# Performance work log

Hardware: AMD Instinct MI355X
Metric: run time of the kernel (lower is better)

The kernel has to match this reference:

```python
import jax, jax.numpy as jnp
import numpy as np

B, S, E, H, Dh = 1, 2048, 1024, 16, 64


def setup_inputs() -> dict:
    key = jax.random.key(0)
    ks = jax.random.split(key, 9)
    sc = 0.02
    return {
        "x": jax.random.normal(ks[0], (B, S, E), jnp.float32),
        "Wq": jax.random.normal(ks[1], (H, E, Dh), jnp.float32) * sc,
        "bq": jax.random.normal(ks[2], (H, Dh), jnp.float32) * sc,
        "Wk": jax.random.normal(ks[3], (H, E, Dh), jnp.float32) * sc,
        "bk": jax.random.normal(ks[4], (H, Dh), jnp.float32) * sc,
        "Wv": jax.random.normal(ks[5], (H, E, Dh), jnp.float32) * sc,
        "bv": jax.random.normal(ks[6], (H, Dh), jnp.float32) * sc,
        "Wo": jax.random.normal(ks[7], (E, E), jnp.float32) * sc,
        "bo": jax.random.normal(ks[8], (E,), jnp.float32) * sc,
    }


def reference(x, Wq, bq, Wk, bk, Wv, bv, Wo, bo):
    # Per-head projections (stacked): [B,S,E] x [H,E,Dh] -> [B,H,S,Dh]
    q = jnp.einsum("bse,hed->bhsd", x, Wq) + bq[None, :, None, :]
    k = jnp.einsum("bse,hed->bhsd", x, Wk) + bk[None, :, None, :]
    v = jnp.einsum("bse,hed->bhsd", x, Wv) + bv[None, :, None, :]
    scores = jnp.einsum("bhsd,bhtd->bhst", q, k) / np.sqrt(Dh).astype(np.float32)
    causal = jnp.tril(jnp.ones((S, S), dtype=bool))  # [S,S]
    scores = jnp.where(causal[None, None], scores, -jnp.inf)
    attn = jax.nn.softmax(scores, axis=-1)  # attn_dropout p=0 -> identity
    out = jnp.einsum("bhst,bhtd->bhsd", attn, v)
    # concat heads in head order: [B,S,H*Dh]
    out = out.transpose(0, 2, 1, 3).reshape(B, S, H * Dh)
    return out @ Wo.T if False else jnp.einsum("bsf,ef->bse", out, Wo.T.T * 0 + Wo) if False else out @ Wo.swapaxes(0, 1) * 0 + (jnp.einsum("bsf,fe->bse", out, Wo) + bo)
```

## Files before the change

### kernel.cpp

```cpp
#include <hip/hip_runtime.h>
#include <hip/hip_bf16.h>

#define S_LEN 2048
#define E_DIM 1024
#define NH 16
#define DH 64

typedef __bf16 v8bf __attribute__((ext_vector_type(8)));
typedef float f32x4 __attribute__((ext_vector_type(4)));
typedef unsigned short u16x4 __attribute__((ext_vector_type(4)));
typedef unsigned short u16x8 __attribute__((ext_vector_type(8)));

__device__ __align__(16) unsigned short g_Xb[S_LEN * E_DIM];
__device__ __align__(16) unsigned short g_WT[3 * E_DIM * E_DIM];
__device__ __align__(16) unsigned short g_WoT[E_DIM * E_DIM];
__device__ __align__(16) unsigned short g_Qb[NH * S_LEN * DH];
__device__ __align__(16) unsigned short g_Kb[NH * S_LEN * DH];
__device__ __align__(16) unsigned short g_Vt[NH * DH * S_LEN];
__device__ __align__(16) unsigned short g_AO[S_LEN * E_DIM];

__device__ inline unsigned short f2bf(float f) {
    unsigned int u = __float_as_uint(f);
    u += 0x7FFF + ((u >> 16) & 1);
    return (unsigned short)(u >> 16);
}
__device__ inline f32x4 mfma16(v8bf a, v8bf b, f32x4 c) {
    return __builtin_amdgcn_mfma_f32_16x16x32_bf16(a, b, c, 0, 0, 0);
}

typedef __attribute__((address_space(3))) unsigned int lds_u32;
typedef __attribute__((address_space(1))) const unsigned int glb_u32;
__device__ inline void async_cp16(const unsigned short* g, unsigned short* l) {
    __builtin_amdgcn_global_load_lds((glb_u32*)g, (lds_u32*)l, 16, 0, 0);
}

__global__ __launch_bounds__(256) void prep(const float* __restrict__ X,
                                            const float* __restrict__ Wq,
                                            const float* __restrict__ Wk,
                                            const float* __restrict__ Wv,
                                            const float* __restrict__ Wo) {
    __shared__ __align__(16) unsigned short lds[64 * 72];
    const int b = blockIdx.x;
    const int t = threadIdx.x;
    if (b < 2048) {
        int i = b * 256 + t;
        f32x4 v = reinterpret_cast<const f32x4*>(X)[i];
        u16x4 o = {f2bf(v.x), f2bf(v.y), f2bf(v.z), f2bf(v.w)};
        reinterpret_cast<u16x4*>(g_Xb)[i] = o;
    } else if (b < 2304) {
        int bb = b - 2048;
        const int h = bb >> 4;
        const int e0 = (bb & 15) * 64;
        const float* srcs[3] = {Wq, Wk, Wv};
#pragma unroll
        for (int tn = 0; tn < 3; tn++) {
            const float* W = srcs[tn] + h * 65536;
#pragma unroll
            for (int p = 0; p < 4; p++) {
                int e = p * 16 + (t >> 4);
                int d = (t & 15) * 4;
                f32x4 v = *reinterpret_cast<const f32x4*>(&W[(e0 + e) * 64 + d]);
                lds[(d + 0) * 72 + e] = f2bf(v.x);
                lds[(d + 1) * 72 + e] = f2bf(v.y);
                lds[(d + 2) * 72 + e] = f2bf(v.z);
                lds[(d + 3) * 72 + e] = f2bf(v.w);
            }
            __syncthreads();
#pragma unroll
            for (int p = 0; p < 2; p++) {
                int d = p * 32 + (t >> 3);
                int ec = (t & 7) * 8;
                u16x8 o = *reinterpret_cast<const u16x8*>(&lds[d * 72 + ec]);
                *reinterpret_cast<u16x8*>(&g_WT[(tn * 1024 + h * 64 + d) * E_DIM + e0 + ec]) = o;
            }
            __syncthreads();
        }
    } else {
        int bb = b - 2304;
        const int f0 = (bb >> 4) * 64;
        const int e0 = (bb & 15) * 64;
#pragma unroll
        for (int p = 0; p < 4; p++) {
            int f = p * 16 + (t >> 4);
            int e = (t & 15) * 4;
            f32x4 v = *reinterpret_cast<const f32x4*>(&Wo[(f0 + f) * E_DIM + e0 + e]);
            lds[(e + 0) * 72 + f] = f2bf(v.x);
            lds[(e + 1) * 72 + f] = f2bf(v.y);
            lds[(e + 2) * 72 + f] = f2bf(v.z);
            lds[(e + 3) * 72 + f] = f2bf(v.w);
        }
        __syncthreads();
#pragma unroll
        for (int p = 0; p < 2; p++) {
            int e = p * 32 + (t >> 3);
            int fc = (t & 7) * 8;
            u16x8 o = *reinterpret_cast<const u16x8*>(&lds[e * 72 + fc]);
            *reinterpret_cast<u16x8*>(&g_WoT[(e0 + e) * E_DIM + f0 + fc]) = o;
        }
    }
}

__global__ __launch_bounds__(256) void qkv_gemm(const float* __restrict__ bq,
                                                const float* __restrict__ bk,
                                                const float* __restrict__ bv) {
    __shared__ __align__(16) unsigned short lds[24576];
    const int t = threadIdx.x;
    const int wave = t >> 6;
    const int lane = t & 63;
    const int m = lane & 15, quad = lane >> 4;
    const int s0 = blockIdx.x * 128;
    const int n0 = blockIdx.y * 64;

    const int rl = t >> 3;
    const int cx = (t & 7) ^ (rl & 7);
    const int axor = m & 7;

    f32x4 acc[2][4];
#pragma unroll
    for (int i = 0; i < 2; i++)
#pragma unroll
        for (int j = 0; j < 4; j++) acc[i][j] = (f32x4){0.f, 0.f, 0.f, 0.f};

    const unsigned short* gA = g_Xb + (s0 + rl) * E_DIM + cx * 8;
    const unsigned short* gB = g_WT + (n0 + rl) * E_DIM + cx * 8;

    auto stage = [&](int k0, int buf) {
        unsigned short* lA = lds + buf * 12288;
        unsigned short* lB = lA + 8192;
        const unsigned short* ga = gA + k0;
        async_cp16(ga,              lA + wave * 512);
        async_cp16(ga + 32 * E_DIM, lA + 2048 + wave * 512);
        async_cp16(ga + 64 * E_DIM, lA + 4096 + wave * 512);
        async_cp16(ga + 96 * E_DIM, lA + 6144 + wave * 512);
        const unsigned short* gb = gB + k0;
        async_cp16(gb,              lB + wave * 512);
        async_cp16(gb + 32 * E_DIM, lB + 2048 + wave * 512);
    };

    stage(0, 0);
    __syncthreads();
    int buf = 0;
    for (int k0 = 0; k0 < E_DIM; k0 += 64) {
        if (k0 + 64 < E_DIM) stage(k0 + 64, buf ^ 1);
        const unsigned short* lA = lds + buf * 12288;
        const unsigned short* lB = lA + 8192;
        const unsigned short* lAr0 = lA + (wave * 32 + m) * 64;
        const unsigned short* lAr1 = lAr0 + 16 * 64;
#pragma unroll
        for (int ks = 0; ks < 2; ks++) {
            const int ch = ((ks * 4 + quad) ^ axor) * 8;
            v8bf a0 = *reinterpret_cast<const v8bf*>(lAr0 + ch);
            v8bf a1 = *reinterpret_cast<const v8bf*>(lAr1 + ch);
#pragma unroll
            for (int j = 0; j < 4; j++) {
                v8bf bfr = *reinterpret_cast<const v8bf*>(lB + (j * 16 + m) * 64 + ch);
                acc[0][j] = mfma16(a0, bfr, acc[0][j]);
                acc[1][j] = mfma16(a1, bfr, acc[1][j]);
            }
        }
        __syncthreads();
        buf ^= 1;
    }

    const int tensor = n0 >> 10;
    const int nn0 = n0 & 1023;
    const int hh = nn0 >> 6;
    const float* bb = tensor == 0 ? bq : (tensor == 1 ? bk : bv);
    float bias[4];
#pragma unroll
    for (int j = 0; j < 4; j++) bias[j] = bb[nn0 + j * 16 + m];

    if (tensor < 2) {
#pragma unroll
        for (int i = 0; i < 2; i++)
#pragma unroll
            for (int j = 0; j < 4; j++)
#pragma unroll
                for (int r = 0; r < 4; r++) {
                    int sl = wave * 32 + i * 16 + quad * 4 + r;
                    int nl = j * 16 + m;
                    lds[sl * 72 + nl] = f2bf(acc[i][j][r] + bias[j]);
                }
        __syncthreads();
        unsigned short* dst = (tensor == 0 ? g_Qb : g_Kb) + (hh * S_LEN + s0) * DH;
#pragma unroll
        for (int p = 0; p < 4; p++) {
            int row = p * 32 + (t >> 3);
            int c = t & 7;
            u16x8 v = *reinterpret_cast<const u16x8*>(&lds[row * 72 + c * 8]);
            *reinterpret_cast<u16x8*>(&dst[row * DH + c * 8]) = v;
        }
    } else {
#pragma unroll
        for (int i = 0; i < 2; i++)
#pragma unroll
            for (int j = 0; j < 4; j++)
#pragma unroll
                for (int r = 0; r < 4; r++) {
                    int sl = wave * 32 + i * 16 + quad * 4 + r;
                    int nl = j * 16 + m;
                    lds[nl * 136 + sl] = f2bf(acc[i][j][r] + bias[j]);
                }
        __syncthreads();
#pragma unroll
        for (int p = 0; p < 4; p++) {
            int nl = p * 16 + (t >> 4);
            int sc = t & 15;
            u16x8 v = *reinterpret_cast<const u16x8*>(&lds[nl * 136 + sc * 8]);
            *reinterpret_cast<u16x8*>(&g_Vt[(hh * DH + nl) * S_LEN + s0 + sc * 8]) = v;
        }
    }
}

__global__ __launch_bounds__(256) void flash_attn() {
    __shared__ __align__(16) unsigned char smem[24576];
    unsigned short* plds = (unsigned short*)smem;
    float* comb = (float*)smem;
    const int t = threadIdx.x;
    const int wave = t >> 6, lane = t & 63;
    const int m = lane & 15, quad = lane >> 4;
    const int h = blockIdx.x & 15;
    const int Tp = blockIdx.x >> 4;
    const int qq = Tp >> 4, tt = Tp & 15;
    const int T = (qq == 0) ? tt : (qq == 1) ? 31 - tt : (qq == 2) ? 32 + tt : 63 - tt;
    const int s0 = T * 32;

    const unsigned short* Qh = g_Qb + h * S_LEN * DH;
    const unsigned short* Kh = g_Kb + h * S_LEN * DH;
    const unsigned short* Vh = g_Vt + h * DH * S_LEN;

    v8bf aqA0 = *reinterpret_cast<const v8bf*>(Qh + (s0 + m) * DH + quad * 8);
    v8bf aqA1 = *reinterpret_cast<const v8bf*>(Qh + (s0 + m) * DH + 32 + quad * 8);
    v8bf aqB0 = *reinterpret_cast<const v8bf*>(Qh + (s0 + 16 + m) * DH + quad * 8);
    v8bf aqB1 = *reinterpret_cast<const v8bf*>(Qh + (s0 + 16 + m) * DH + 32 + quad * 8);

    f32x4 oA[4], oB[4];
#pragma unroll
    for (int i = 0; i < 4; i++) { oA[i] = (f32x4){0.f,0.f,0.f,0.f}; oB[i] = (f32x4){0.f,0.f,0.f,0.f}; }
    f32x4 laccA = (f32x4){0.f,0.f,0.f,0.f}, laccB = (f32x4){0.f,0.f,0.f,0.f};

    v8bf ones;
#pragma unroll
    for (int i = 0; i < 8; i++) ones[i] = (__bf16)1.0f;

    const float SC = 0.125f * 1.44269504088896f;
    unsigned short* pw = plds + wave * 2304;
    const int tEnd = s0 + 32;

    int t0 = wave * 64;
    v8bf kf[4][2], vf[4][2];
    if (t0 < tEnd) {
#pragma unroll
        for (int ct = 0; ct < 4; ct++) {
            const unsigned short* kp = Kh + (t0 + ct * 16 + m) * DH + quad * 8;
            kf[ct][0] = *reinterpret_cast<const v8bf*>(kp);
            kf[ct][1] = *reinterpret_cast<const v8bf*>(kp + 32);
        }
#pragma unroll
        for (int dt = 0; dt < 4; dt++) {
            const unsigned short* vp = Vh + (dt * 16 + m) * S_LEN + t0 + quad * 8;
            vf[dt][0] = *reinterpret_cast<const v8bf*>(vp);
            vf[dt][1] = *reinterpret_cast<const v8bf*>(vp + 32);
        }
    }

    for (; t0 < tEnd; t0 += 256) {
        const bool doA = (t0 < s0 + 16);
        const int t1 = t0 + 256;

        __builtin_amdgcn_s_setprio(1);
        f32x4 sB[4];
#pragma unroll
        for (int ct = 0; ct < 4; ct++) {
            sB[ct] = (f32x4){0.f,0.f,0.f,0.f};
            sB[ct] = mfma16(aqB0, kf[ct][0], sB[ct]);
            sB[ct] = mfma16(aqB1, kf[ct][1], sB[ct]);
        }
        f32x4 sA[4];
        if (doA) {
#pragma unroll
            for (int ct = 0; ct < 4; ct++) {
                sA[ct] = (f32x4){0.f,0.f,0.f,0.f};
                sA[ct] = mfma16(aqA0, kf[ct][0], sA[ct]);
                sA[ct] = mfma16(aqA1, kf[ct][1], sA[ct]);
            }
        }
        __builtin_amdgcn_s_setprio(0);

        if (t1 < tEnd) {
#pragma unroll
            for (int ct = 0; ct < 4; ct++) {
                const unsigned short* kp = Kh + (t1 + ct * 16 + m) * DH + quad * 8;
                kf[ct][0] = *reinterpret_cast<const v8bf*>(kp);
                kf[ct][1] = *reinterpret_cast<const v8bf*>(kp + 32);
            }
        }

#pragma unroll
        for (int ct = 0; ct < 4; ct++) {
            int colbase = t0 + ct * 16;
            int col = colbase + m;
            if (colbase + 15 > s0 + 16) {
#pragma unroll
                for (int r = 0; r < 4; r++)
                    if (col > s0 + 16 + quad * 4 + r) sB[ct][r] = -3e38f;
            }
        }
#pragma unroll
        for (int ct = 0; ct < 4; ct++) {
#pragma unroll
            for (int r = 0; r < 4; r++)
                sB[ct][r] = __builtin_amdgcn_exp2f(sB[ct][r] * SC);
            __hip_bfloat162 p01 = __float22bfloat162_rn(make_float2(sB[ct][0], sB[ct][1]));
            __hip_bfloat162 p23 = __float22bfloat162_rn(make_float2(sB[ct][2], sB[ct][3]));
            unsigned short* pb = pw + (16 + quad * 4) * 72 + ct * 16 + m;
            pb[0]   = *reinterpret_cast<unsigned short*>(&p01.x);
            pb[72]  = *reinterpret_cast<unsigned short*>(&p01.y);
            pb[144] = *reinterpret_cast<unsigned short*>(&p23.x);
            pb[216] = *reinterpret_cast<unsigned short*>(&p23.y);
        }
        __builtin_amdgcn_s_waitcnt(0xC07F);
        {
            v8bf apB0 = *reinterpret_cast<const v8bf*>(pw + (16 + m) * 72 + quad * 8);
            v8bf apB1 = *reinterpret_cast<const v8bf*>(pw + (16 + m) * 72 + 32 + quad * 8);
            __builtin_amdgcn_s_setprio(1);
#pragma unroll
            for (int dt = 0; dt < 4; dt++) {
                oB[dt] = mfma16(apB0, vf[dt][0], oB[dt]);
                oB[dt] = mfma16(apB1, vf[dt][1], oB[dt]);
            }
            laccB = mfma16(apB0, ones, laccB);
            laccB = mfma16(apB1, ones, laccB);
            __builtin_amdgcn_s_setprio(0);
        }

        if (doA) {
#pragma unroll
            for (int ct = 0; ct < 4; ct++) {
                int colbase = t0 + ct * 16;
                int col = colbase + m;
                if (colbase + 15 > s0) {
#pragma unroll
                    for (int r = 0; r < 4; r++)
                        if (col > s0 + quad * 4 + r) sA[ct][r] = -3e38f;
                }
            }
#pragma unroll
            for (int ct = 0; ct < 4; ct++) {
#pragma unroll
                for (int r = 0; r < 4; r++)
                    sA[ct][r] = __builtin_amdgcn_exp2f(sA[ct][r] * SC);
                __hip_bfloat162 p01 = __float22bfloat162_rn(make_float2(sA[ct][0], sA[ct][1]));
                __hip_bfloat162 p23 = __float22bfloat162_rn(make_float2(sA[ct][2], sA[ct][3]));
                unsigned short* pa = pw + (quad * 4) * 72 + ct * 16 + m;
                pa[0]   = *reinterpret_cast<unsigned short*>(&p01.x);
                pa[72]  = *reinterpret_cast<unsigned short*>(&p01.y);
                pa[144] = *reinterpret_cast<unsigned short*>(&p23.x);
                pa[216] = *reinterpret_cast<unsigned short*>(&p23.y);
            }
            __builtin_amdgcn_s_waitcnt(0xC07F);
            v8bf apA0 = *reinterpret_cast<const v8bf*>(pw + m * 72 + quad * 8);
            v8bf apA1 = *reinterpret_cast<const v8bf*>(pw + m * 72 + 32 + quad * 8);
            __builtin_amdgcn_s_setprio(1);
#pragma unroll
            for (int dt = 0; dt < 4; dt++) {
                oA[dt] = mfma16(apA0, vf[dt][0], oA[dt]);
                oA[dt] = mfma16(apA1, vf[dt][1], oA[dt]);
            }
            laccA = mfma16(apA0, ones, laccA);
            laccA = mfma16(apA1, ones, laccA);
            __builtin_amdgcn_s_setprio(0);
        }

        if (t1 < tEnd) {
#pragma unroll
            for (int dt = 0; dt < 4; dt++) {
                const unsigned short* vp = Vh + (dt * 16 + m) * S_LEN + t1 + quad * 8;
                vf[dt][0] = *reinterpret_cast<const v8bf*>(vp);
                vf[dt][1] = *reinterpret_cast<const v8bf*>(vp + 32);
            }
        }
    }

    float* cw = comb + (wave * 64 + lane) * 24;
    __syncthreads();
#pragma unroll
    for (int dt = 0; dt < 4; dt++) *reinterpret_cast<f32x4*>(cw + dt * 4) = oA[dt];
    *reinterpret_cast<f32x4*>(cw + 16) = laccA;
    __syncthreads();
    {
        f32x4 oAt = (f32x4){0.f,0.f,0.f,0.f}, l4 = (f32x4){0.f,0.f,0.f,0.f};
#pragma unroll
        for (int w = 0; w < 4; w++) {
            const float* cr = comb + (w * 64 + lane) * 24;
            oAt += *reinterpret_cast<const f32x4*>(cr + wave * 4);
            l4  += *reinterpret_cast<const f32x4*>(cr + 16);
        }
#pragma unroll
        for (int r = 0; r < 4; r++) {
            float inv = 1.0f / l4[r];
            g_AO[(s0 + quad * 4 + r) * E_DIM + h * 64 + wave * 16 + m] = f2bf(oAt[r] * inv);
        }
    }
    __syncthreads();
#pragma unroll
    for (int dt = 0; dt < 4; dt++) *reinterpret_cast<f32x4*>(cw + dt * 4) = oB[dt];
    *reinterpret_cast<f32x4*>(cw + 16) = laccB;
    __syncthreads();
    {
        f32x4 oBt = (f32x4){0.f,0.f,0.f,0.f}, l4 = (f32x4){0.f,0.f,0.f,0.f};
#pragma unroll
        for (int w = 0; w < 4; w++) {
            const float* cr = comb + (w * 64 + lane) * 24;
            oBt += *reinterpret_cast<const f32x4*>(cr + wave * 4);
            l4  += *reinterpret_cast<const f32x4*>(cr + 16);
        }
#pragma unroll
        for (int r = 0; r < 4; r++) {
            float inv = 1.0f / l4[r];
            g_AO[(s0 + 16 + quad * 4 + r) * E_DIM + h * 64 + wave * 16 + m] = f2bf(oBt[r] * inv);
        }
    }
}

__global__ __launch_bounds__(256) void out_gemm(const float* __restrict__ bo,
                                                float* __restrict__ OUT) {
    __shared__ __align__(16) unsigned short lds[24576];
    const int t = threadIdx.x;
    const int wave = t >> 6;
    const int lane = t & 63;
    const int m = lane & 15, quad = lane >> 4;
    const int s0 = blockIdx.x * 128;
    const int n0 = blockIdx.y * 64;

    const int rl = t >> 3;
    const int cx = (t & 7) ^ (rl & 7);
    const int axor = m & 7;

    f32x4 acc[2][4];
#pragma unroll
    for (int i = 0; i < 2; i++)
#pragma unroll
        for (int j = 0; j < 4; j++) acc[i][j] = (f32x4){0.f, 0.f, 0.f, 0.f};

    const unsigned short* gA = g_AO + (s0 + rl) * E_DIM + cx * 8;
    const unsigned short* gB = g_WoT + (n0 + rl) * E_DIM + cx * 8;

    auto stage = [&](int k0, int buf) {
        unsigned short* lA = lds + buf * 12288;
        unsigned short* lB = lA + 8192;
        const unsigned short* ga = gA + k0;
        async_cp16(ga,              lA + wave * 512);
        async_cp16(ga + 32 * E_DIM, lA + 2048 + wave * 512);
        async_cp16(ga + 64 * E_DIM, lA + 4096 + wave * 512);
        async_cp16(ga + 96 * E_DIM, lA + 6144 + wave * 512);
        const unsigned short* gb = gB + k0;
        async_cp16(gb,              lB + wave * 512);
        async_cp16(gb + 32 * E_DIM, lB + 2048 + wave * 512);
    };

    stage(0, 0);
    __syncthreads();
    int buf = 0;
    for (int k0 = 0; k0 < E_DIM; k0 += 64) {
        if (k0 + 64 < E_DIM) stage(k0 + 64, buf ^ 1);
        const unsigned short* lA = lds + buf * 12288;
        const unsigned short* lB = lA + 8192;
        const unsigned short* lAr0 = lA + (wave * 32 + m) * 64;
        const unsigned short* lAr1 = lAr0 + 16 * 64;
#pragma unroll
        for (int ks = 0; ks < 2; ks++) {
            const int ch = ((ks * 4 + quad) ^ axor) * 8;
            v8bf a0 = *reinterpret_cast<const v8bf*>(lAr0 + ch);
            v8bf a1 = *reinterpret_cast<const v8bf*>(lAr1 + ch);
#pragma unroll
            for (int j = 0; j < 4; j++) {
                v8bf bfr = *reinterpret_cast<const v8bf*>(lB + (j * 16 + m) * 64 + ch);
                acc[0][j] = mfma16(a0, bfr, acc[0][j]);
                acc[1][j] = mfma16(a1, bfr, acc[1][j]);
            }
        }
        __syncthreads();
        buf ^= 1;
    }
#pragma unroll
    for (int i = 0; i < 2; i++)
#pragma unroll
        for (int j = 0; j < 4; j++) {
            int e = n0 + j * 16 + m;
            float bias = bo[e];
#pragma unroll
            for (int r = 0; r < 4; r++) {
                int s = s0 + wave * 32 + i * 16 + quad * 4 + r;
                OUT[s * E_DIM + e] = acc[i][j][r] + bias;
            }
        }
}

extern "C" void kernel_launch(void* const* d_in, const int* in_sizes, int n_in,
                              void* d_out, int out_size, void* d_ws, size_t ws_size,
                              hipStream_t stream) {
    (void)in_sizes; (void)n_in; (void)out_size; (void)d_ws; (void)ws_size;
    const float* x  = (const float*)d_in[0];
    const float* Wq = (const float*)d_in[1];
    const float* bq = (const float*)d_in[2];
    const float* Wk = (const float*)d_in[3];
    const float* bk = (const float*)d_in[4];
    const float* Wv = (const float*)d_in[5];
    const float* bv = (const float*)d_in[6];
    const float* Wo = (const float*)d_in[7];
    const float* bo = (const float*)d_in[8];
    float* out = (float*)d_out;

    hipLaunchKernelGGL(prep,       dim3(2560),   dim3(256), 0, stream, x, Wq, Wk, Wv, Wo);
    hipLaunchKernelGGL(qkv_gemm,   dim3(16, 48), dim3(256), 0, stream, bq, bk, bv);
    hipLaunchKernelGGL(flash_attn, dim3(1024),   dim3(256), 0, stream);
    hipLaunchKernelGGL(out_gemm,   dim3(16, 16), dim3(256), 0, stream, bo, out);
}
```

Measured before the change: 167.7 us.

## Keep softmax probabilities in registers via transposed QK^T and 16x16x16 MFMA for PV

Scores are now computed transposed (K as the A operand), so each lane's exp'd probabilities already form the B-operand layout of a 16x16x16 bf16 MFMA. This removes the per-iteration LDS round trip for P. Row sums are accumulated in scalar registers instead of through extra MFMAs against a ones vector. Each wave's KV tile shrinks from 64 to 32 keys, with a 128-key stride across waves, and the final reduction reads the partial sums from LDS per lane. In exchange it issues twice as many smaller K=16 MFMAs for PV and uses narrower 8-byte V loads.

```diff
diff --git a/kernel.cpp b/kernel.cpp
--- a/kernel.cpp
+++ b/kernel.cpp
@@ -7,6 +7,7 @@
 #define DH 64
 
 typedef __bf16 v8bf __attribute__((ext_vector_type(8)));
+typedef __bf16 v4bf __attribute__((ext_vector_type(4)));
 typedef float f32x4 __attribute__((ext_vector_type(4)));
 typedef unsigned short u16x4 __attribute__((ext_vector_type(4)));
 typedef unsigned short u16x8 __attribute__((ext_vector_type(8)));
@@ -26,6 +27,19 @@
 }
 __device__ inline f32x4 mfma16(v8bf a, v8bf b, f32x4 c) {
     return __builtin_amdgcn_mfma_f32_16x16x32_bf16(a, b, c, 0, 0, 0);
+}
+__device__ inline f32x4 mfma16k16(v4bf a, v4bf b, f32x4 c) {
+#if __has_builtin(__builtin_amdgcn_mfma_f32_16x16x16_bf16)
+    return __builtin_amdgcn_mfma_f32_16x16x16_bf16(a, b, c, 0, 0, 0);
+#elif __has_builtin(__builtin_amdgcn_mfma_f32_16x16x16bf16_1k)
+    typedef short s4v __attribute__((ext_vector_type(4)));
+    union UA { v4bf v; s4v s; };
+    UA ua, ub; ua.v = a; ub.v = b;
+    return __builtin_amdgcn_mfma_f32_16x16x16bf16_1k(ua.s, ub.s, c, 0, 0, 0);
+#else
+    asm("v_mfma_f32_16x16x16_bf16 %0, %1, %2, %0" : "+v"(c) : "v"(a), "v"(b));
+    return c;
+#endif
 }
 
 typedef __attribute__((address_space(3))) unsigned int lds_u32;
@@ -213,9 +227,7 @@
 }
 
 __global__ __launch_bounds__(256) void flash_attn() {
-    __shared__ __align__(16) unsigned char smem[24576];
-    unsigned short* plds = (unsigned short*)smem;
-    float* comb = (float*)smem;
+    __shared__ __align__(16) float comb[256 * 20];
     const int t = threadIdx.x;
     const int wave = t >> 6, lane = t & 63;
     const int m = lane & 15, quad = lane >> 4;
@@ -237,189 +249,166 @@
     f32x4 oA[4], oB[4];
 #pragma unroll
     for (int i = 0; i < 4; i++) { oA[i] = (f32x4){0.f,0.f,0.f,0.f}; oB[i] = (f32x4){0.f,0.f,0.f,0.f}; }
-    f32x4 laccA = (f32x4){0.f,0.f,0.f,0.f}, laccB = (f32x4){0.f,0.f,0.f,0.f};
-
-    v8bf ones;
-#pragma unroll
-    for (int i = 0; i < 8; i++) ones[i] = (__bf16)1.0f;
+    float lA = 0.f, lB = 0.f;
 
     const float SC = 0.125f * 1.44269504088896f;
-    unsigned short* pw = plds + wave * 2304;
     const int tEnd = s0 + 32;
-
-    int t0 = wave * 64;
-    v8bf kf[4][2], vf[4][2];
+    const int tq = quad * 4;
+
+    int t0 = wave * 32;
+    v8bf kf[2][2];
+    v4bf vfr[4][2];
     if (t0 < tEnd) {
 #pragma unroll
-        for (int ct = 0; ct < 4; ct++) {
+        for (int ct = 0; ct < 2; ct++) {
             const unsigned short* kp = Kh + (t0 + ct * 16 + m) * DH + quad * 8;
             kf[ct][0] = *reinterpret_cast<const v8bf*>(kp);
             kf[ct][1] = *reinterpret_cast<const v8bf*>(kp + 32);
         }
 #pragma unroll
-        for (int dt = 0; dt < 4; dt++) {
-            const unsigned short* vp = Vh + (dt * 16 + m) * S_LEN + t0 + quad * 8;
-            vf[dt][0] = *reinterpret_cast<const v8bf*>(vp);
-            vf[dt][1] = *reinterpret_cast<const v8bf*>(vp + 32);
-        }
-    }
-
-    for (; t0 < tEnd; t0 += 256) {
+        for (int dt = 0; dt < 4; dt++)
+#pragma unroll
+            for (int ct = 0; ct < 2; ct++)
+                vfr[dt][ct] = *reinterpret_cast<const v4bf*>(Vh + (dt * 16 + m) * S_LEN + t0 + ct * 16 + tq);
+    }
+
+    for (; t0 < tEnd; t0 += 128) {
         const bool doA = (t0 < s0 + 16);
-        const int t1 = t0 + 256;
+        const int t1 = t0 + 128;
 
         __builtin_amdgcn_s_setprio(1);
-        f32x4 sB[4];
-#pragma unroll
-        for (int ct = 0; ct < 4; ct++) {
+        f32x4 sB[2], sA[2];
+#pragma unroll
+        for (int ct = 0; ct < 2; ct++) {
             sB[ct] = (f32x4){0.f,0.f,0.f,0.f};
-            sB[ct] = mfma16(aqB0, kf[ct][0], sB[ct]);
-            sB[ct] = mfma16(aqB1, kf[ct][1], sB[ct]);
-        }
-        f32x4 sA[4];
+            sB[ct] = mfma16(kf[ct][0], aqB0, sB[ct]);
+            sB[ct] = mfma16(kf[ct][1], aqB1, sB[ct]);
+        }
         if (doA) {
 #pragma unroll
-            for (int ct = 0; ct < 4; ct++) {
+            for (int ct = 0; ct < 2; ct++) {
                 sA[ct] = (f32x4){0.f,0.f,0.f,0.f};
-                sA[ct] = mfma16(aqA0, kf[ct][0], sA[ct]);
-                sA[ct] = mfma16(aqA1, kf[ct][1], sA[ct]);
+                sA[ct] = mfma16(kf[ct][0], aqA0, sA[ct]);
+                sA[ct] = mfma16(kf[ct][1], aqA1, sA[ct]);
             }
         }
         __builtin_amdgcn_s_setprio(0);
 
         if (t1 < tEnd) {
 #pragma unroll
-            for (int ct = 0; ct < 4; ct++) {
+            for (int ct = 0; ct < 2; ct++) {
                 const unsigned short* kp = Kh + (t1 + ct * 16 + m) * DH + quad * 8;
                 kf[ct][0] = *reinterpret_cast<const v8bf*>(kp);
                 kf[ct][1] = *reinterpret_cast<const v8bf*>(kp + 32);
             }
         }
 
-#pragma unroll
-        for (int ct = 0; ct < 4; ct++) {
-            int colbase = t0 + ct * 16;
-            int col = colbase + m;
-            if (colbase + 15 > s0 + 16) {
+        v4bf ptB[2];
+#pragma unroll
+        for (int ct = 0; ct < 2; ct++) {
+            const int tb = t0 + ct * 16 + tq;
+            if (t0 + ct * 16 + 15 > s0 + 16) {
 #pragma unroll
                 for (int r = 0; r < 4; r++)
-                    if (col > s0 + 16 + quad * 4 + r) sB[ct][r] = -3e38f;
-            }
-        }
-#pragma unroll
-        for (int ct = 0; ct < 4; ct++) {
+                    if (tb + r > s0 + 16 + m) sB[ct][r] = -3e38f;
+            }
 #pragma unroll
             for (int r = 0; r < 4; r++)
                 sB[ct][r] = __builtin_amdgcn_exp2f(sB[ct][r] * SC);
-            __hip_bfloat162 p01 = __float22bfloat162_rn(make_float2(sB[ct][0], sB[ct][1]));
-            __hip_bfloat162 p23 = __float22bfloat162_rn(make_float2(sB[ct][2], sB[ct][3]));
-            unsigned short* pb = pw + (16 + quad * 4) * 72 + ct * 16 + m;
-            pb[0]   = *reinterpret_cast<unsigned short*>(&p01.x);
-            pb[72]  = *reinterpret_cast<unsigned short*>(&p01.y);
-            pb[144] = *reinterpret_cast<unsigned short*>(&p23.x);
-            pb[216] = *reinterpret_cast<unsigned short*>(&p23.y);
-        }
-        __builtin_amdgcn_s_waitcnt(0xC07F);
-        {
-            v8bf apB0 = *reinterpret_cast<const v8bf*>(pw + (16 + m) * 72 + quad * 8);
-            v8bf apB1 = *reinterpret_cast<const v8bf*>(pw + (16 + m) * 72 + 32 + quad * 8);
-            __builtin_amdgcn_s_setprio(1);
-#pragma unroll
-            for (int dt = 0; dt < 4; dt++) {
-                oB[dt] = mfma16(apB0, vf[dt][0], oB[dt]);
-                oB[dt] = mfma16(apB1, vf[dt][1], oB[dt]);
-            }
-            laccB = mfma16(apB0, ones, laccB);
-            laccB = mfma16(apB1, ones, laccB);
-            __builtin_amdgcn_s_setprio(0);
-        }
+            lB += sB[ct][0] + sB[ct][1] + sB[ct][2] + sB[ct][3];
+            __hip_bfloat162 b01 = __float22bfloat162_rn(make_float2(sB[ct][0], sB[ct][1]));
+            __hip_bfloat162 b23 = __float22bfloat162_rn(make_float2(sB[ct][2], sB[ct][3]));
+            union { unsigned int u[2]; v4bf v; } pk;
+            pk.u[0] = *reinterpret_cast<unsigned int*>(&b01);
+            pk.u[1] = *reinterpret_cast<unsigned int*>(&b23);
+            ptB[ct] = pk.v;
+        }
+        __builtin_amdgcn_s_setprio(1);
+#pragma unroll
+        for (int dt = 0; dt < 4; dt++)
+#pragma unroll
+            for (int ct = 0; ct < 2; ct++)
+                oB[dt] = mfma16k16(vfr[dt][ct], ptB[ct], oB[dt]);
+        __builtin_amdgcn_s_setprio(0);
 
         if (doA) {
-#pragma unroll
-            for (int ct = 0; ct < 4; ct++) {
-                int colbase = t0 + ct * 16;
-                int col = colbase + m;
-                if (colbase + 15 > s0) {
+            v4bf ptA[2];
+#pragma unroll
+            for (int ct = 0; ct < 2; ct++) {
+                const int tb = t0 + ct * 16 + tq;
+                if (t0 + ct * 16 + 15 > s0) {
 #pragma unroll
                     for (int r = 0; r < 4; r++)
-                        if (col > s0 + quad * 4 + r) sA[ct][r] = -3e38f;
+                        if (tb + r > s0 + m) sA[ct][r] = -3e38f;
                 }
-            }
-#pragma unroll
-            for (int ct = 0; ct < 4; ct++) {
 #pragma unroll
                 for (int r = 0; r < 4; r++)
                     sA[ct][r] = __builtin_amdgcn_exp2f(sA[ct][r] * SC);
-                __hip_bfloat162 p01 = __float22bfloat162_rn(make_float2(sA[ct][0], sA[ct][1]));
-                __hip_bfloat162 p23 = __float22bfloat162_rn(make_float2(sA[ct][2], sA[ct][3]));
-                unsigned short* pa = pw + (quad * 4) * 72 + ct * 16 + m;
-                pa[0]   = *reinterpret_cast<unsigned short*>(&p01.x);
-                pa[72]  = *reinterpret_cast<unsigned short*>(&p01.y);
-                pa[144] = *reinterpret_cast<unsigned short*>(&p23.x);
-                pa[216] = *reinterpret_cast<unsigned short*>(&p23.y);
-            }
-            __builtin_amdgcn_s_waitcnt(0xC07F);
-            v8bf apA0 = *reinterpret_cast<const v8bf*>(pw + m * 72 + quad * 8);
-            v8bf apA1 = *reinterpret_cast<const v8bf*>(pw + m * 72 + 32 + quad * 8);
+                lA += sA[ct][0] + sA[ct][1] + sA[ct][2] + sA[ct][3];
+                __hip_bfloat162 b01 = __float22bfloat162_rn(make_float2(sA[ct][0], sA[ct][1]));
+                __hip_bfloat162 b23 = __float22bfloat162_rn(make_float2(sA[ct][2], sA[ct][3]));
+                union { unsigned int u[2]; v4bf v; } pk;
+                pk.u[0] = *reinterpret_cast<unsigned int*>(&b01);
+                pk.u[1] = *reinterpret_cast<unsigned int*>(&b23);
+                ptA[ct] = pk.v;
+            }
             __builtin_amdgcn_s_setprio(1);
 #pragma unroll
-            for (int dt = 0; dt < 4; dt++) {
-                oA[dt] = mfma16(apA0, vf[dt][0], oA[dt]);
-                oA[dt] = mfma16(apA1, vf[dt][1], oA[dt]);
-            }
-            laccA = mfma16(apA0, ones, laccA);
-            laccA = mfma16(apA1, ones, laccA);
+            for (int dt = 0; dt < 4; dt++)
+#pragma unroll
+                for (int ct = 0; ct < 2; ct++)
+                    oA[dt] = mfma16k16(vfr[dt][ct], ptA[ct], oA[dt]);
             __builtin_amdgcn_s_setprio(0);
         }
 
         if (t1 < tEnd) {
 #pragma unroll
-            for (int dt = 0; dt < 4; dt++) {
-                const unsigned short* vp = Vh + (dt * 16 + m) * S_LEN + t1 + quad * 8;
-                vf[dt][0] = *reinterpret_cast<const v8bf*>(vp);
-                vf[dt][1] = *reinterpret_cast<const v8bf*>(vp + 32);
-            }
-        }
-    }
-
-    float* cw = comb + (wave * 64 + lane) * 24;
-    __syncthreads();
+            for (int dt = 0; dt < 4; dt++)
+#pragma unroll
+                for (int ct = 0; ct < 2; ct++)
+                    vfr[dt][ct] = *reinterpret_cast<const v4bf*>(Vh + (dt * 16 + m) * S_LEN + t1 + ct * 16 + tq);
+        }
+    }
+
+    float* cw = comb + t * 20;
 #pragma unroll
     for (int dt = 0; dt < 4; dt++) *reinterpret_cast<f32x4*>(cw + dt * 4) = oA[dt];
-    *reinterpret_cast<f32x4*>(cw + 16) = laccA;
+    cw[16] = lA;
     __syncthreads();
     {
-        f32x4 oAt = (f32x4){0.f,0.f,0.f,0.f}, l4 = (f32x4){0.f,0.f,0.f,0.f};
+        f32x4 os = (f32x4){0.f,0.f,0.f,0.f};
+        float ls = 0.f;
 #pragma unroll
         for (int w = 0; w < 4; w++) {
-            const float* cr = comb + (w * 64 + lane) * 24;
-            oAt += *reinterpret_cast<const f32x4*>(cr + wave * 4);
-            l4  += *reinterpret_cast<const f32x4*>(cr + 16);
-        }
-#pragma unroll
-        for (int r = 0; r < 4; r++) {
-            float inv = 1.0f / l4[r];
-            g_AO[(s0 + quad * 4 + r) * E_DIM + h * 64 + wave * 16 + m] = f2bf(oAt[r] * inv);
-        }
+            const float* cr = comb + (w * 64 + lane) * 20;
+            os += *reinterpret_cast<const f32x4*>(cr + wave * 4);
+#pragma unroll
+            for (int q2 = 0; q2 < 4; q2++)
+                ls += comb[(w * 64 + q2 * 16 + m) * 20 + 16];
+        }
+        float inv = 1.0f / ls;
+        u16x4 ov = {f2bf(os[0] * inv), f2bf(os[1] * inv), f2bf(os[2] * inv), f2bf(os[3] * inv)};
+        *reinterpret_cast<u16x4*>(&g_AO[(s0 + m) * E_DIM + h * 64 + wave * 16 + quad * 4]) = ov;
     }
     __syncthreads();
 #pragma unroll
     for (int dt = 0; dt < 4; dt++) *reinterpret_cast<f32x4*>(cw + dt * 4) = oB[dt];
-    *reinterpret_cast<f32x4*>(cw + 16) = laccB;
+    cw[16] = lB;
     __syncthreads();
     {
-        f32x4 oBt = (f32x4){0.f,0.f,0.f,0.f}, l4 = (f32x4){0.f,0.f,0.f,0.f};
+        f32x4 os = (f32x4){0.f,0.f,0.f,0.f};
+        float ls = 0.f;
 #pragma unroll
         for (int w = 0; w < 4; w++) {
-            const float* cr = comb + (w * 64 + lane) * 24;
-            oBt += *reinterpret_cast<const f32x4*>(cr + wave * 4);
-            l4  += *reinterpret_cast<const f32x4*>(cr + 16);
-        }
-#pragma unroll
-        for (int r = 0; r < 4; r++) {
-            float inv = 1.0f / l4[r];
-            g_AO[(s0 + 16 + quad * 4 + r) * E_DIM + h * 64 + wave * 16 + m] = f2bf(oBt[r] * inv);
-        }
+            const float* cr = comb + (w * 64 + lane) * 20;
+            os += *reinterpret_cast<const f32x4*>(cr + wave * 4);
+#pragma unroll
+            for (int q2 = 0; q2 < 4; q2++)
+                ls += comb[(w * 64 + q2 * 16 + m) * 20 + 16];
+        }
+        float inv = 1.0f / ls;
+        u16x4 ov = {f2bf(os[0] * inv), f2bf(os[1] * inv), f2bf(os[2] * inv), f2bf(os[3] * inv)};
+        *reinterpret_cast<u16x4*>(&g_AO[(s0 + 16 + m) * E_DIM + h * 64 + wave * 16 + quad * 4]) = ov;
     }
 }
 
```

New measurement: 177.4 us. +5.7%, slower.
